# Kernel optimization log

Hardware: AMD Instinct MI355X
Metric: run time of the kernel (lower is better)

Reference implementation:

```python
import jax, jax.numpy as jnp
import numpy as np

EPS = 1e-8  # torch cosine_similarity default eps


def setup_inputs() -> dict:
    key = jax.random.key(0)
    k1, k2, k3 = jax.random.split(key, 3)
    bsz, sent_len, cont_dim, mp_dim = 16, 512, 768, 20
    repres = jax.random.normal(k1, (bsz, sent_len, cont_dim), dtype=jnp.float32)
    max_att = jax.random.normal(k2, (bsz, sent_len, cont_dim), dtype=jnp.float32)
    # nn.Parameter initialized uniform_(-1, 1)
    weight = jax.random.uniform(k3, (mp_dim, cont_dim), dtype=jnp.float32, minval=-1.0, maxval=1.0)
    return {"repres": repres, "max_att": max_att, "weight": weight}


def reference(repres, max_att, weight):
    # Original math: a = repres[:,None,:] * w[None], b = max_att[:,None,:] * w[None]
    # cos = <a,b> / (max(||a||,eps) * max(||b||,eps)) along last dim.
    # Fused form: never materialize [N, mp_dim, cont_dim]; contract with w^2 directly.
    bsz, sent_len, cont_dim = repres.shape
    r = repres.reshape(-1, cont_dim)   # [N, D]
    m = max_att.reshape(-1, cont_dim)  # [N, D]
    w2 = weight * weight               # [P, D]
    dot = jnp.einsum('nd,pd->np', r * m, w2)              # [N, P]
    n1 = jnp.sqrt(jnp.einsum('nd,pd->np', r * r, w2))     # [N, P]
    n2 = jnp.sqrt(jnp.einsum('nd,pd->np', m * m, w2))     # [N, P]
    cos = dot / (jnp.maximum(n1, EPS) * jnp.maximum(n2, EPS))
    return cos.reshape(bsz, sent_len, weight.shape[0])
```

## Files before the change

### kernel.cpp

```cpp
#include <hip/hip_runtime.h>
#include <math.h>
#include <stdint.h>

static constexpr int D_DIM   = 768;
static constexpr int NP      = 20;
static constexpr int NROWS   = 8192;
static constexpr int ROWS_PB = 16;
static constexpr int BLOCKS  = NROWS / ROWS_PB;
static constexpr int KW      = 192;
static constexpr int KSLICE  = 32;
static constexpr int NSLICES = KW / KSLICE;

typedef short  short8  __attribute__((ext_vector_type(8)));
typedef float  float4v __attribute__((ext_vector_type(4)));

static constexpr int A_WAVE = 8192;
static constexpr int A_BUF  = 4096;
static constexpr int A_MAT  = 2048;
static constexpr int B_OFF  = 32768;
static constexpr int B_CSTR = 776 * 2;
static constexpr int LDS_SZ = B_OFF + NP * B_CSTR;

__device__ __forceinline__ void async_copy16(const void* g, void* l) {
  __builtin_amdgcn_global_load_lds(
      (const __attribute__((address_space(1))) unsigned int*)(uintptr_t)g,
      (__attribute__((address_space(3))) unsigned int*)(uint32_t)(uintptr_t)l,
      16, 0, 0);
}

__device__ __forceinline__ unsigned short bf16_rne(float x) {
  unsigned u = __float_as_uint(x);
  u += 0x7FFFu + ((u >> 16) & 1u);
  return (unsigned short)(u >> 16);
}
__device__ __forceinline__ float bf16f(unsigned short h) {
  return __uint_as_float(((unsigned)h) << 16);
}

__global__ __launch_bounds__(256) void atte_cos_mfma(
    const float* __restrict__ repres,
    const float* __restrict__ max_att,
    const float* __restrict__ weight,
    float* __restrict__ out)
{
  const int tid  = threadIdx.x;
  const int wave = tid >> 6;
  const int lane = tid & 63;
  const int row0 = blockIdx.x * ROWS_PB;
  const int k0   = wave * KW;
  const int part = lane >> 4;
  const int mrow = lane & 15;

  __shared__ __align__(16) char smem[LDS_SZ];
  char* a_base = smem + wave * A_WAVE;

  auto stage = [&](int s, int b) {
#pragma unroll
    for (int j = 0; j < 2; ++j) {
      const int slot = j * 64 + lane;
      const int row  = slot >> 3;
      const int gp   = slot & 7;
      const int gl   = (gp - 2 * (row & 3)) & 7;
      const float* gr = repres  + (size_t)(row0 + row) * D_DIM + k0 + s * KSLICE + gl * 4;
      const float* gm = max_att + (size_t)(row0 + row) * D_DIM + k0 + s * KSLICE + gl * 4;
      char* la = a_base + b * A_BUF + slot * 16;
      async_copy16(gr, la);
      async_copy16(gm, la + A_MAT);
    }
  };

  stage(0, 0);
  stage(1, 1);

  for (int col = 0; col < NP; ++col) {
#pragma unroll
    for (int j = 0; j < 3; ++j) {
      const int k = j * 256 + tid;
      const float wv = weight[col * D_DIM + k];
      *(unsigned short*)(smem + B_OFF + col * B_CSTR + k * 2) = bf16_rne(wv * wv);
    }
  }

  __syncthreads();

  const int a_off = mrow * 128 + (((part + (mrow & 3)) & 3) * 32);
  const char* b0p = smem + B_OFF + (lane & 15) * B_CSTR + (k0 + part * 8) * 2;
  const int c1col = min(16 + (lane & 15), NP - 1);
  const char* b1p = smem + B_OFF + c1col * B_CSTR + (k0 + part * 8) * 2;

  float4v acc[6] = {};

#pragma unroll
  for (int s = 0; s < NSLICES; ++s) {
    __builtin_amdgcn_s_waitcnt(0x0F74);
    const char* ab = a_base + (s & 1) * A_BUF;

    float rv[8], mv[8];
    *(float4*)&rv[0] = *(const float4*)(ab + a_off);
    *(float4*)&rv[4] = *(const float4*)(ab + a_off + 16);
    *(float4*)&mv[0] = *(const float4*)(ab + A_MAT + a_off);
    *(float4*)&mv[4] = *(const float4*)(ab + A_MAT + a_off + 16);

    short8 a0h, a0l, a1h, a2h;
#pragma unroll
    for (int j = 0; j < 8; ++j) {
      const float pm = rv[j] * mv[j];
      const float pr = rv[j] * rv[j];
      const float pq = mv[j] * mv[j];
      const unsigned short h = bf16_rne(pm);
      a0h[j] = (short)h;
      a0l[j] = (short)bf16_rne(pm - bf16f(h));
      a1h[j] = (short)bf16_rne(pr);
      a2h[j] = (short)bf16_rne(pq);
    }

    const short8 b0 = *(const short8*)(b0p + s * 64);
    const short8 b1 = *(const short8*)(b1p + s * 64);

    acc[0] = __builtin_amdgcn_mfma_f32_16x16x32_bf16(a0h, b0, acc[0], 0, 0, 0);
    acc[0] = __builtin_amdgcn_mfma_f32_16x16x32_bf16(a0l, b0, acc[0], 0, 0, 0);
    acc[1] = __builtin_amdgcn_mfma_f32_16x16x32_bf16(a0h, b1, acc[1], 0, 0, 0);
    acc[1] = __builtin_amdgcn_mfma_f32_16x16x32_bf16(a0l, b1, acc[1], 0, 0, 0);
    acc[2] = __builtin_amdgcn_mfma_f32_16x16x32_bf16(a1h, b0, acc[2], 0, 0, 0);
    acc[3] = __builtin_amdgcn_mfma_f32_16x16x32_bf16(a1h, b1, acc[3], 0, 0, 0);
    acc[4] = __builtin_amdgcn_mfma_f32_16x16x32_bf16(a2h, b0, acc[4], 0, 0, 0);
    acc[5] = __builtin_amdgcn_mfma_f32_16x16x32_bf16(a2h, b1, acc[5], 0, 0, 0);

    if (s + 2 < NSLICES) {
      __builtin_amdgcn_s_waitcnt(0xC07F);
      stage(s + 2, s & 1);
    }
  }

  __syncthreads();
#pragma unroll
  for (int qc = 0; qc < 6; ++qc)
    *(float4v*)(smem + ((qc * 4 + wave) * 64 + lane) * 16) = acc[qc];
  __syncthreads();

  if (wave < 2) {
    const int ct = wave;
    float4v c0 = {}, c1 = {}, c2 = {};
#pragma unroll
    for (int wv = 0; wv < 4; ++wv) {
      c0 += *(const float4v*)(smem + (((0 * 2 + ct) * 4 + wv) * 64 + lane) * 16);
      c1 += *(const float4v*)(smem + (((1 * 2 + ct) * 4 + wv) * 64 + lane) * 16);
      c2 += *(const float4v*)(smem + (((2 * 2 + ct) * 4 + wv) * 64 + lane) * 16);
    }
    const int col = ct * 16 + (lane & 15);
    if (col < NP) {
      const int rbase = row0 + (lane >> 4) * 4;
#pragma unroll
      for (int r = 0; r < 4; ++r) {
        const float n1 = fmaxf(sqrtf(c1[r]), 1e-8f);
        const float n2 = fmaxf(sqrtf(c2[r]), 1e-8f);
        out[(size_t)(rbase + r) * NP + col] = c0[r] / (n1 * n2);
      }
    }
  }
}

extern "C" void kernel_launch(void* const* d_in, const int* in_sizes, int n_in,
                              void* d_out, int out_size, void* d_ws, size_t ws_size,
                              hipStream_t stream) {
  const float* repres  = (const float*)d_in[0];
  const float* max_att = (const float*)d_in[1];
  const float* weight  = (const float*)d_in[2];
  float* out = (float*)d_out;

  atte_cos_mfma<<<BLOCKS, 256, 0, stream>>>(repres, max_att, weight, out);
}
```

Before: 89.34 us.

## Load A and squared-weight operands directly into registers, dropping LDS staging

Replaces the async global-to-LDS double-buffered staging of repres/max_att and the block-wide LDS table of squared bf16 weights with direct per-lane vectorized global loads into registers. Each lane now loads its own weight slices and squares and converts them locally, and all input slices are issued up front. LDS use shrinks to the reduction scratch, and launch bounds request two blocks per CU to raise occupancy. The cost is higher register pressure, redundant weight loads and conversions per wave, and less coalesced row-strided global access patterns.

```diff
diff --git a/kernel.cpp b/kernel.cpp
--- a/kernel.cpp
+++ b/kernel.cpp
@@ -8,25 +8,10 @@
 static constexpr int ROWS_PB = 16;
 static constexpr int BLOCKS  = NROWS / ROWS_PB;
 static constexpr int KW      = 192;
-static constexpr int KSLICE  = 32;
-static constexpr int NSLICES = KW / KSLICE;
+static constexpr int NSLICES = 6;
 
 typedef short  short8  __attribute__((ext_vector_type(8)));
 typedef float  float4v __attribute__((ext_vector_type(4)));
-
-static constexpr int A_WAVE = 8192;
-static constexpr int A_BUF  = 4096;
-static constexpr int A_MAT  = 2048;
-static constexpr int B_OFF  = 32768;
-static constexpr int B_CSTR = 776 * 2;
-static constexpr int LDS_SZ = B_OFF + NP * B_CSTR;
-
-__device__ __forceinline__ void async_copy16(const void* g, void* l) {
-  __builtin_amdgcn_global_load_lds(
-      (const __attribute__((address_space(1))) unsigned int*)(uintptr_t)g,
-      (__attribute__((address_space(3))) unsigned int*)(uint32_t)(uintptr_t)l,
-      16, 0, 0);
-}
 
 __device__ __forceinline__ unsigned short bf16_rne(float x) {
   unsigned u = __float_as_uint(x);
@@ -37,7 +22,7 @@
   return __uint_as_float(((unsigned)h) << 16);
 }
 
-__global__ __launch_bounds__(256) void atte_cos_mfma(
+__global__ __launch_bounds__(256, 2) void atte_cos_mfma(
     const float* __restrict__ repres,
     const float* __restrict__ max_att,
     const float* __restrict__ weight,
@@ -51,55 +36,59 @@
   const int part = lane >> 4;
   const int mrow = lane & 15;
 
-  __shared__ __align__(16) char smem[LDS_SZ];
-  char* a_base = smem + wave * A_WAVE;
+  __shared__ __align__(16) float4v scratch[6][4][64];
 
-  auto stage = [&](int s, int b) {
+  const int kbase = k0 + part * 8;
+  const float* ra = repres  + (size_t)(row0 + mrow) * D_DIM + kbase;
+  const float* ma = max_att + (size_t)(row0 + mrow) * D_DIM + kbase;
+  const int col0 = mrow;
+  const int col1 = (16 + mrow < NP) ? 16 + mrow : NP - 1;
+  const float* wb0 = weight + (size_t)col0 * D_DIM + kbase;
+  const float* wb1 = weight + (size_t)col1 * D_DIM + kbase;
+
+  float4 ar[NSLICES][2], am[NSLICES][2];
 #pragma unroll
-    for (int j = 0; j < 2; ++j) {
-      const int slot = j * 64 + lane;
-      const int row  = slot >> 3;
-      const int gp   = slot & 7;
-      const int gl   = (gp - 2 * (row & 3)) & 7;
-      const float* gr = repres  + (size_t)(row0 + row) * D_DIM + k0 + s * KSLICE + gl * 4;
-      const float* gm = max_att + (size_t)(row0 + row) * D_DIM + k0 + s * KSLICE + gl * 4;
-      char* la = a_base + b * A_BUF + slot * 16;
-      async_copy16(gr, la);
-      async_copy16(gm, la + A_MAT);
-    }
-  };
+  for (int s = 0; s < 2; ++s) {
+    ar[s][0] = *(const float4*)(ra + s * 32);
+    ar[s][1] = *(const float4*)(ra + s * 32 + 4);
+    am[s][0] = *(const float4*)(ma + s * 32);
+    am[s][1] = *(const float4*)(ma + s * 32 + 4);
+  }
+  float4 wf0[NSLICES][2], wf1[NSLICES][2];
+#pragma unroll
+  for (int s = 0; s < NSLICES; ++s) {
+    wf0[s][0] = *(const float4*)(wb0 + s * 32);
+    wf0[s][1] = *(const float4*)(wb0 + s * 32 + 4);
+    wf1[s][0] = *(const float4*)(wb1 + s * 32);
+    wf1[s][1] = *(const float4*)(wb1 + s * 32 + 4);
+  }
 
-  stage(0, 0);
-  stage(1, 1);
-
-  for (int col = 0; col < NP; ++col) {
+  short8 b0r[NSLICES], b1r[NSLICES];
 #pragma unroll
-    for (int j = 0; j < 3; ++j) {
-      const int k = j * 256 + tid;
-      const float wv = weight[col * D_DIM + k];
-      *(unsigned short*)(smem + B_OFF + col * B_CSTR + k * 2) = bf16_rne(wv * wv);
+  for (int s = 0; s < NSLICES; ++s) {
+    const float* f0 = (const float*)&wf0[s][0];
+    const float* f1 = (const float*)&wf1[s][0];
+#pragma unroll
+    for (int j = 0; j < 8; ++j) {
+      b0r[s][j] = (short)bf16_rne(f0[j] * f0[j]);
+      b1r[s][j] = (short)bf16_rne(f1[j] * f1[j]);
     }
   }
 
-  __syncthreads();
-
-  const int a_off = mrow * 128 + (((part + (mrow & 3)) & 3) * 32);
-  const char* b0p = smem + B_OFF + (lane & 15) * B_CSTR + (k0 + part * 8) * 2;
-  const int c1col = min(16 + (lane & 15), NP - 1);
-  const char* b1p = smem + B_OFF + c1col * B_CSTR + (k0 + part * 8) * 2;
+#pragma unroll
+  for (int s = 2; s < NSLICES; ++s) {
+    ar[s][0] = *(const float4*)(ra + s * 32);
+    ar[s][1] = *(const float4*)(ra + s * 32 + 4);
+    am[s][0] = *(const float4*)(ma + s * 32);
+    am[s][1] = *(const float4*)(ma + s * 32 + 4);
+  }
 
   float4v acc[6] = {};
 
 #pragma unroll
   for (int s = 0; s < NSLICES; ++s) {
-    __builtin_amdgcn_s_waitcnt(0x0F74);
-    const char* ab = a_base + (s & 1) * A_BUF;
-
-    float rv[8], mv[8];
-    *(float4*)&rv[0] = *(const float4*)(ab + a_off);
-    *(float4*)&rv[4] = *(const float4*)(ab + a_off + 16);
-    *(float4*)&mv[0] = *(const float4*)(ab + A_MAT + a_off);
-    *(float4*)&mv[4] = *(const float4*)(ab + A_MAT + a_off + 16);
+    const float* rv = (const float*)&ar[s][0];
+    const float* mv = (const float*)&am[s][0];
 
     short8 a0h, a0l, a1h, a2h;
 #pragma unroll
@@ -114,28 +103,19 @@
       a2h[j] = (short)bf16_rne(pq);
     }
 
-    const short8 b0 = *(const short8*)(b0p + s * 64);
-    const short8 b1 = *(const short8*)(b1p + s * 64);
-
-    acc[0] = __builtin_amdgcn_mfma_f32_16x16x32_bf16(a0h, b0, acc[0], 0, 0, 0);
-    acc[0] = __builtin_amdgcn_mfma_f32_16x16x32_bf16(a0l, b0, acc[0], 0, 0, 0);
-    acc[1] = __builtin_amdgcn_mfma_f32_16x16x32_bf16(a0h, b1, acc[1], 0, 0, 0);
-    acc[1] = __builtin_amdgcn_mfma_f32_16x16x32_bf16(a0l, b1, acc[1], 0, 0, 0);
-    acc[2] = __builtin_amdgcn_mfma_f32_16x16x32_bf16(a1h, b0, acc[2], 0, 0, 0);
-    acc[3] = __builtin_amdgcn_mfma_f32_16x16x32_bf16(a1h, b1, acc[3], 0, 0, 0);
-    acc[4] = __builtin_amdgcn_mfma_f32_16x16x32_bf16(a2h, b0, acc[4], 0, 0, 0);
-    acc[5] = __builtin_amdgcn_mfma_f32_16x16x32_bf16(a2h, b1, acc[5], 0, 0, 0);
-
-    if (s + 2 < NSLICES) {
-      __builtin_amdgcn_s_waitcnt(0xC07F);
-      stage(s + 2, s & 1);
-    }
+    acc[0] = __builtin_amdgcn_mfma_f32_16x16x32_bf16(a0h, b0r[s], acc[0], 0, 0, 0);
+    acc[0] = __builtin_amdgcn_mfma_f32_16x16x32_bf16(a0l, b0r[s], acc[0], 0, 0, 0);
+    acc[1] = __builtin_amdgcn_mfma_f32_16x16x32_bf16(a0h, b1r[s], acc[1], 0, 0, 0);
+    acc[1] = __builtin_amdgcn_mfma_f32_16x16x32_bf16(a0l, b1r[s], acc[1], 0, 0, 0);
+    acc[2] = __builtin_amdgcn_mfma_f32_16x16x32_bf16(a1h, b0r[s], acc[2], 0, 0, 0);
+    acc[3] = __builtin_amdgcn_mfma_f32_16x16x32_bf16(a1h, b1r[s], acc[3], 0, 0, 0);
+    acc[4] = __builtin_amdgcn_mfma_f32_16x16x32_bf16(a2h, b0r[s], acc[4], 0, 0, 0);
+    acc[5] = __builtin_amdgcn_mfma_f32_16x16x32_bf16(a2h, b1r[s], acc[5], 0, 0, 0);
   }
 
-  __syncthreads();
 #pragma unroll
   for (int qc = 0; qc < 6; ++qc)
-    *(float4v*)(smem + ((qc * 4 + wave) * 64 + lane) * 16) = acc[qc];
+    scratch[qc][wave][lane] = acc[qc];
   __syncthreads();
 
   if (wave < 2) {
@@ -143,9 +123,9 @@
     float4v c0 = {}, c1 = {}, c2 = {};
 #pragma unroll
     for (int wv = 0; wv < 4; ++wv) {
-      c0 += *(const float4v*)(smem + (((0 * 2 + ct) * 4 + wv) * 64 + lane) * 16);
-      c1 += *(const float4v*)(smem + (((1 * 2 + ct) * 4 + wv) * 64 + lane) * 16);
-      c2 += *(const float4v*)(smem + (((2 * 2 + ct) * 4 + wv) * 64 + lane) * 16);
+      c0 += scratch[0 * 2 + ct][wv][lane];
+      c1 += scratch[1 * 2 + ct][wv][lane];
+      c2 += scratch[2 * 2 + ct][wv][lane];
     }
     const int col = ct * 16 + (lane & 15);
     if (col < NP) {
```

After: 92.81 us. 1.04x slower.
